# Kernel tuning notes

Measured on AMD Instinct MI355X. Metric: run time of the kernel, lower is better.

## Reference

```python
import jax, jax.numpy as jnp
import numpy as np

GROUPS = 8
NUM_HEADS = 4
EPS = 1e-5

def setup_inputs() -> dict:
    key = jax.random.key(0)
    k1, k2, k3 = jax.random.split(key, 3)
    B, C, H, W = 4, 128, 64, 64
    x = jax.random.normal(k1, (B, C, H, W), dtype=jnp.float32)
    gn_w = jnp.ones((C,), jnp.float32)
    gn_b = jnp.zeros((C,), jnp.float32)
    qkv_w = jax.random.normal(k2, (3 * C, C), dtype=jnp.float32) * (1.0 / np.sqrt(C))
    qkv_b = jnp.zeros((3 * C,), jnp.float32)
    proj_w = jax.random.normal(k3, (C, C), dtype=jnp.float32) * (1.0 / np.sqrt(C))
    proj_b = jnp.zeros((C,), jnp.float32)
    return {"x": x, "gn_w": gn_w, "gn_b": gn_b, "qkv_w": qkv_w,
            "qkv_b": qkv_b, "proj_w": proj_w, "proj_b": proj_b}

def group_norm(x, w, b):
    B, C, H, W = x.shape
    xg = x.reshape(B, GROUPS, C // GROUPS, H, W)
    mean = jnp.mean(xg, axis=(2, 3, 4), keepdims=True)
    var = jnp.var(xg, axis=(2, 3, 4), keepdims=True)
    xn = ((xg - mean) * jax.lax.rsqrt(var + EPS)).reshape(B, C, H, W)
    return xn * w[None, :, None, None] + b[None, :, None, None]

def reference(x, gn_w, gn_b, qkv_w, qkv_b, proj_w, proj_b):
    B, C, H, W = x.shape
    nh = NUM_HEADS
    hd = C // nh
    xn = group_norm(x, gn_w, gn_b)  # residual is the NORMALIZED x (torch code reassigns x)
    # 1x1 conv == channel matmul
    qkv = jnp.einsum('oc,bchw->bohw', qkv_w, xn) + qkv_b[None, :, None, None]
    qkv = qkv.reshape(B, 3, nh, hd, H * W)
    q, k, v = qkv[:, 0], qkv[:, 1], qkv[:, 2]          # [B, nh, hd, HW]
    attn = jnp.einsum('bhcd,bhce->bhde', q, k) * (C ** -0.5)  # note: full-C scale, as in torch code
    attn = jax.nn.softmax(attn, axis=-1)
    out = jnp.einsum('bhde,bhce->bhcd', attn, v).reshape(B, C, H, W)
    out = jnp.einsum('oc,bchw->bohw', proj_w, out) + proj_b[None, :, None, None]
    return out + xn
```

## Files before the change

### kernel.cpp

```cpp
#include <hip/hip_runtime.h>
#include <math.h>

#define BATCH 4
#define C 128
#define HW 4096
#define G 8
#define CPG 16
#define NH 4
#define HD 32
#define EPS 1e-5f
#define SCALE 0.08838834764831845f
#define LOG2E 1.44269504088896340f
#define GP 136

typedef unsigned int uint;
typedef unsigned short ushort;
typedef __attribute__((ext_vector_type(8))) short bf16x8;
typedef __attribute__((ext_vector_type(4))) float f32x4;

__device__ __forceinline__ ushort f2bf(float x) {
  uint u = __float_as_uint(x);
  u += 0x7fff + ((u >> 16) & 1);
  return (ushort)(u >> 16);
}
__device__ __forceinline__ ushort f2bf_r(float x) {
  return (ushort)((__float_as_uint(x) + 0x8000u) >> 16);
}
__device__ __forceinline__ float bf2f(ushort h) {
  return __uint_as_float(((uint)h) << 16);
}
__device__ __forceinline__ uint pk(float a, float b) {
#if __has_builtin(__builtin_amdgcn_cvt_pk_bf16_f32)
  auto r = __builtin_amdgcn_cvt_pk_bf16_f32(a, b);
  union { decltype(r) v; uint u; } x;
  x.v = r;
  return x.u;
#else
  uint ua = __float_as_uint(a) + 0x8000u;
  uint ub = __float_as_uint(b) + 0x8000u;
  return __builtin_amdgcn_perm(ub, ua, 0x07060302);
#endif
}
__device__ __forceinline__ bf16x8 as_bf(uint4 u) {
  union { uint4 a; bf16x8 b; } x; x.a = u; return x.b;
}
__device__ __forceinline__ float fexp2(float x) {
#if __has_builtin(__builtin_amdgcn_exp2f)
  return __builtin_amdgcn_exp2f(x);
#else
  return __exp2f(x);
#endif
}

__global__ __launch_bounds__(256) void gn_part(
    const float* __restrict__ x, float* __restrict__ stats) {
  const int bg = blockIdx.x >> 3, chunk = blockIdx.x & 7;
  const float* xp = x + (size_t)bg * (CPG * HW) + chunk * 8192;
  const int tid = threadIdx.x;
  float s = 0.f, ss = 0.f;
  #pragma unroll
  for (int j = 0; j < 8; j++) {
    float4 v = ((const float4*)xp)[j * 256 + tid];
    s += (v.x + v.y) + (v.z + v.w);
    ss += (v.x * v.x + v.y * v.y) + (v.z * v.z + v.w * v.w);
  }
  #pragma unroll
  for (int off = 32; off; off >>= 1) {
    s  += __shfl_down(s, off);
    ss += __shfl_down(ss, off);
  }
  __shared__ float rs[4], rss[4];
  const int lane = tid & 63, wid = tid >> 6;
  if (lane == 0) { rs[wid] = s; rss[wid] = ss; }
  __syncthreads();
  if (tid == 0) {
    stats[(bg * 8 + chunk) * 2]     = (rs[0] + rs[1]) + (rs[2] + rs[3]);
    stats[(bg * 8 + chunk) * 2 + 1] = (rss[0] + rss[1]) + (rss[2] + rss[3]);
  }
}

__device__ __forceinline__ void gn_coeff(
    const float* __restrict__ stats, const float* __restrict__ w,
    const float* __restrict__ b, int batch, int c, float& ca, float& cb) {
  const int bg = batch * G + (c >> 4);
  float s = 0.f, ss = 0.f;
  #pragma unroll
  for (int k = 0; k < 8; k++) {
    s  += stats[(bg * 8 + k) * 2];
    ss += stats[(bg * 8 + k) * 2 + 1];
  }
  const float mean = s * (1.0f / 65536.0f);
  const float var  = ss * (1.0f / 65536.0f) - mean * mean;
  const float inv  = rsqrtf(var + EPS);
  ca = w[c] * inv;
  cb = b[c] - mean * ca;
}

__global__ __launch_bounds__(256) void qkv_gemm(
    const float* __restrict__ x, const float* __restrict__ stats,
    const float* __restrict__ gnw, const float* __restrict__ gnb,
    const float* __restrict__ w, const float* __restrict__ bias,
    ushort* __restrict__ qkvb, ushort* __restrict__ kt) {
  const int b = blockIdx.z, my = blockIdx.y, n0 = blockIdx.x * 64;
  const int m0 = my * 128;
  const int tid = threadIdx.x, lane = tid & 63, wv = tid >> 6;
  const int li = lane & 15, g = lane >> 4;
  __shared__ ushort Ws[128][GP];
  __shared__ ushort Xs[64][GP];
  __shared__ float CA[C], CB[C];

  if (tid < C) gn_coeff(stats, gnw, gnb, b, tid, CA[tid], CB[tid]);
  __syncthreads();

  {
    const int row = tid >> 2, c0 = (tid & 3) * 32;
    #pragma unroll
    for (int mh = 0; mh < 2; mh++) {
      const float* wr = w + (size_t)(m0 + mh * 64 + row) * C + c0;
      #pragma unroll
      for (int k = 0; k < 4; k++) {
        float4 f0 = ((const float4*)wr)[k * 2];
        float4 f1 = ((const float4*)wr)[k * 2 + 1];
        uint4 u = {pk(f0.x, f0.y), pk(f0.z, f0.w), pk(f1.x, f1.y), pk(f1.z, f1.w)};
        *(uint4*)&Ws[mh * 64 + row][c0 + k * 8] = u;
      }
    }
  }
  {
    const int nX = tid & 63, c0 = (tid >> 6) * 32;
    const float* xb = x + (size_t)(b * C + c0) * HW + n0 + nX;
    #pragma unroll
    for (int k = 0; k < 4; k++) {
      float xv[8];
      #pragma unroll
      for (int j = 0; j < 8; j++) {
        int c = c0 + k * 8 + j;
        xv[j] = fmaf(xb[(size_t)(k * 8 + j) * HW], CA[c], CB[c]);
      }
      uint4 u = {pk(xv[0], xv[1]), pk(xv[2], xv[3]), pk(xv[4], xv[5]), pk(xv[6], xv[7])};
      *(uint4*)&Xs[nX][c0 + k * 8] = u;
    }
  }
  __syncthreads();

  f32x4 acc[2][4];
  #pragma unroll
  for (int mh = 0; mh < 2; mh++)
    #pragma unroll
    for (int nt = 0; nt < 4; nt++) acc[mh][nt] = (f32x4){0.f, 0.f, 0.f, 0.f};
  #pragma unroll
  for (int kk = 0; kk < 4; kk++) {
    bf16x8 af0 = *(const bf16x8*)&Ws[wv * 16 + li][kk * 32 + g * 8];
    bf16x8 af1 = *(const bf16x8*)&Ws[64 + wv * 16 + li][kk * 32 + g * 8];
    #pragma unroll
    for (int nt = 0; nt < 4; nt++) {
      bf16x8 bfr = *(const bf16x8*)&Xs[nt * 16 + li][kk * 32 + g * 8];
      acc[0][nt] = __builtin_amdgcn_mfma_f32_16x16x32_bf16(af0, bfr, acc[0][nt], 0, 0, 0);
      acc[1][nt] = __builtin_amdgcn_mfma_f32_16x16x32_bf16(af1, bfr, acc[1][nt], 0, 0, 0);
    }
  }
  #pragma unroll
  for (int mh = 0; mh < 2; mh++) {
    const int ob = m0 + mh * 64 + wv * 16 + g * 4;
    if (my == 1) {
      const int ck = ob - C;
      const int h  = ck >> 5;
      const int cl = ck & 31;
      ushort* ktp = kt + (size_t)(b * NH + h) * HW * HD;
      #pragma unroll
      for (int r = 0; r < 4; r++) {
        float bi = bias[ob + r];
        #pragma unroll
        for (int nt = 0; nt < 4; nt++) {
          int e = n0 + nt * 16 + li;
          ktp[(size_t)e * HD + cl + r] = f2bf(acc[mh][nt][r] + bi);
        }
      }
    } else {
      #pragma unroll
      for (int r = 0; r < 4; r++) {
        float bi = bias[ob + r];
        #pragma unroll
        for (int nt = 0; nt < 4; nt++) {
          qkvb[(size_t)(b * 3 * C + ob + r) * HW + n0 + nt * 16 + li] = f2bf(acc[mh][nt][r] + bi);
        }
      }
    }
  }
}

__global__ __launch_bounds__(512, 4) void attn_kernel(
    ushort* __restrict__ qkv, const ushort* __restrict__ kt) {
  const int bh = blockIdx.y, b = bh >> 2, h = bh & 3;
  const int tid = threadIdx.x, lane = tid & 63, wv = tid >> 6;
  const int li = lane & 15, g = lane >> 4;
  const int grp = wv >> 2, w4 = wv & 3;
  ushort* qp = qkv + (size_t)(b * 3 * C + h * HD) * HW;
  const ushort* vpl = qkv + (size_t)(b * 3 * C + 2 * C + h * HD) * HW;
  const ushort* ktp = kt + (size_t)bh * HW * HD;
  const int d0 = blockIdx.x * 128 + w4 * 32;

  __shared__ ushort Ks[2][2][32][40];
  __shared__ ushort Vs[2][2][32][40];
  __shared__ float OP[8][64][19];

  const float qs = SCALE * LOG2E;
  bf16x8 qf[2];
  #pragma unroll
  for (int dt = 0; dt < 2; dt++) {
    int d = d0 + dt * 16 + li;
    float qv[8];
    #pragma unroll
    for (int j = 0; j < 8; j++)
      qv[j] = bf2f(qp[(size_t)(g * 8 + j) * HW + d]) * qs;
    uint4 qu = {pk(qv[0], qv[1]), pk(qv[2], qv[3]), pk(qv[4], qv[5]), pk(qv[6], qv[7])};
    qf[dt] = as_bf(qu);
  }

  f32x4 O[2][2];
  #pragma unroll
  for (int dt = 0; dt < 2; dt++)
    #pragma unroll
    for (int ct = 0; ct < 2; ct++) O[dt][ct] = (f32x4){0.f, 0.f, 0.f, 0.f};
  f32x4 lacc[2] = {(f32x4){0.f, 0.f, 0.f, 0.f}, (f32x4){0.f, 0.f, 0.f, 0.f}};
  const uint one2 = 0x3F803F80u;
  const bf16x8 ones = as_bf((uint4){one2, one2, one2, one2});

  const int gt = tid & 255;
  const bool isK = gt < 128;
  const int t2 = gt & 127;
  const int srow = t2 >> 2, scol8 = (t2 & 3) * 8;
  const ushort* gK = ktp + (size_t)(grp * 64) * 1024 + t2 * 8;
  const ushort* gV = vpl + (size_t)srow * HW + grp * 2048 + scol8;

  uint4 st = isK ? *(const uint4*)&gK[0] : *(const uint4*)&gV[0];
  if (isK) *(uint4*)&Ks[grp][0][srow][scol8] = st;
  else     *(uint4*)&Vs[grp][0][srow][scol8] = st;
  st = isK ? *(const uint4*)&gK[1024] : *(const uint4*)&gV[32];
  __syncthreads();

  for (int it = 0; it < 64; it++) {
    const int cur = it & 1, nxt = cur ^ 1;
    if (isK) *(uint4*)&Ks[grp][nxt][srow][scol8] = st;
    else     *(uint4*)&Vs[grp][nxt][srow][scol8] = st;

    bf16x8 kf0 = *(const bf16x8*)&Ks[grp][cur][li][g * 8];
    bf16x8 kf1 = *(const bf16x8*)&Ks[grp][cur][16 + li][g * 8];
    uint2 va0 = *(const uint2*)&Vs[grp][cur][li][4 * g];
    uint2 va1 = *(const uint2*)&Vs[grp][cur][li][16 + 4 * g];
    uint2 vb0 = *(const uint2*)&Vs[grp][cur][16 + li][4 * g];
    uint2 vb1 = *(const uint2*)&Vs[grp][cur][16 + li][16 + 4 * g];
    bf16x8 vf0 = as_bf((uint4){va0.x, va0.y, va1.x, va1.y});
    bf16x8 vf1 = as_bf((uint4){vb0.x, vb0.y, vb1.x, vb1.y});

    const int tn = (it + 2) & 63;
    st = isK ? *(const uint4*)&gK[(size_t)tn * 1024] : *(const uint4*)&gV[tn * 32];

    const f32x4 z = (f32x4){0.f, 0.f, 0.f, 0.f};
    #pragma unroll
    for (int dt = 0; dt < 2; dt++) {
      f32x4 s0 = __builtin_amdgcn_mfma_f32_16x16x32_bf16(kf0, qf[dt], z, 0, 0, 0);
      f32x4 s1 = __builtin_amdgcn_mfma_f32_16x16x32_bf16(kf1, qf[dt], z, 0, 0, 0);
      float p0 = fexp2(s0[0]), p1 = fexp2(s0[1]), p2 = fexp2(s0[2]), p3 = fexp2(s0[3]);
      float p4 = fexp2(s1[0]), p5 = fexp2(s1[1]), p6 = fexp2(s1[2]), p7 = fexp2(s1[3]);
      uint4 pu = {pk(p0, p1), pk(p2, p3), pk(p4, p5), pk(p6, p7)};
      bf16x8 pf = as_bf(pu);
      lacc[dt] = __builtin_amdgcn_mfma_f32_16x16x32_bf16(ones, pf, lacc[dt], 0, 0, 0);
      O[dt][0] = __builtin_amdgcn_mfma_f32_16x16x32_bf16(vf0, pf, O[dt][0], 0, 0, 0);
      O[dt][1] = __builtin_amdgcn_mfma_f32_16x16x32_bf16(vf1, pf, O[dt][1], 0, 0, 0);
    }
    __syncthreads();
  }

  #pragma unroll
  for (int dt = 0; dt < 2; dt++) {
    #pragma unroll
    for (int ct = 0; ct < 2; ct++)
      #pragma unroll
      for (int r = 0; r < 4; r++) OP[wv][lane][dt * 8 + ct * 4 + r] = O[dt][ct][r];
    OP[wv][lane][16 + dt] = lacc[dt][0];
  }
  __syncthreads();
  const int pw = wv ^ 4;
  #pragma unroll
  for (int dt = 0; dt < 2; dt++) {
    const float inv = 1.0f / (lacc[dt][0] + OP[pw][lane][16 + dt]);
    const int d = d0 + dt * 16 + li;
    #pragma unroll
    for (int r = 0; r < 4; r++) {
      float val = O[dt][grp][r] + OP[pw][lane][dt * 8 + grp * 4 + r];
      qp[(size_t)(grp * 16 + g * 4 + r) * HW + d] = f2bf_r(val * inv);
    }
  }
}

__global__ __launch_bounds__(256) void proj_gemm(
    const ushort* __restrict__ qkvb, const float* __restrict__ w,
    const float* __restrict__ bias, const float* __restrict__ x,
    const float* __restrict__ stats, const float* __restrict__ gnw,
    const float* __restrict__ gnb, float* __restrict__ out) {
  const int b = blockIdx.z, m0 = blockIdx.y * 64, n0 = blockIdx.x * 64;
  const int tid = threadIdx.x, lane = tid & 63, wv = tid >> 6;
  const int li = lane & 15, g = lane >> 4;
  __shared__ ushort Ws[64][GP];
  __shared__ ushort Xs[64][GP];
  __shared__ float CA[64], CB[64];

  if (tid < 64) gn_coeff(stats, gnw, gnb, b, m0 + tid, CA[tid], CB[tid]);

  {
    const int row = tid >> 2, c0 = (tid & 3) * 32;
    const float* wr = w + (size_t)(m0 + row) * C + c0;
    #pragma unroll
    for (int k = 0; k < 4; k++) {
      float4 f0 = ((const float4*)wr)[k * 2];
      float4 f1 = ((const float4*)wr)[k * 2 + 1];
      uint4 u = {pk(f0.x, f0.y), pk(f0.z, f0.w), pk(f1.x, f1.y), pk(f1.z, f1.w)};
      *(uint4*)&Ws[row][c0 + k * 8] = u;
    }
  }
  {
    const int nX = tid & 63, c0 = (tid >> 6) * 32;
    const ushort* xb = qkvb + (size_t)(b * 3 * C + c0) * HW + n0 + nX;
    #pragma unroll
    for (int k = 0; k < 4; k++) {
      ushort t8[8];
      #pragma unroll
      for (int j = 0; j < 8; j++) t8[j] = xb[(size_t)(k * 8 + j) * HW];
      uint4 u;
      u.x = t8[0] | ((uint)t8[1] << 16);
      u.y = t8[2] | ((uint)t8[3] << 16);
      u.z = t8[4] | ((uint)t8[5] << 16);
      u.w = t8[6] | ((uint)t8[7] << 16);
      *(uint4*)&Xs[nX][c0 + k * 8] = u;
    }
  }
  __syncthreads();

  f32x4 acc[4];
  #pragma unroll
  for (int nt = 0; nt < 4; nt++) acc[nt] = (f32x4){0.f, 0.f, 0.f, 0.f};
  #pragma unroll
  for (int kk = 0; kk < 4; kk++) {
    bf16x8 af = *(const bf16x8*)&Ws[wv * 16 + li][kk * 32 + g * 8];
    #pragma unroll
    for (int nt = 0; nt < 4; nt++) {
      bf16x8 bfr = *(const bf16x8*)&Xs[nt * 16 + li][kk * 32 + g * 8];
      acc[nt] = __builtin_amdgcn_mfma_f32_16x16x32_bf16(af, bfr, acc[nt], 0, 0, 0);
    }
  }
  const int ob = m0 + wv * 16 + g * 4;
  #pragma unroll
  for (int r = 0; r < 4; r++) {
    const float bi = bias[ob + r];
    const float ca = CA[wv * 16 + g * 4 + r], cb = CB[wv * 16 + g * 4 + r];
    #pragma unroll
    for (int nt = 0; nt < 4; nt++) {
      size_t idx = (size_t)(b * C + ob + r) * HW + n0 + nt * 16 + li;
      out[idx] = acc[nt][r] + bi + fmaf(x[idx], ca, cb);
    }
  }
}

extern "C" void kernel_launch(void* const* d_in, const int* in_sizes, int n_in,
                              void* d_out, int out_size, void* d_ws, size_t ws_size,
                              hipStream_t stream) {
  const float* x     = (const float*)d_in[0];
  const float* gn_w  = (const float*)d_in[1];
  const float* gn_b  = (const float*)d_in[2];
  const float* qkv_w = (const float*)d_in[3];
  const float* qkv_b = (const float*)d_in[4];
  const float* pw    = (const float*)d_in[5];
  const float* pb    = (const float*)d_in[6];
  float* out = (float*)d_out;

  float*  stats = (float*)d_ws;
  ushort* qkvb  = (ushort*)((char*)d_ws + 4096);
  ushort* kt    = qkvb + (size_t)BATCH * 3 * C * HW;

  gn_part<<<dim3(256), dim3(256), 0, stream>>>(x, stats);
  qkv_gemm<<<dim3(HW / 64, 3, BATCH), dim3(256), 0, stream>>>(
      x, stats, gn_w, gn_b, qkv_w, qkv_b, qkvb, kt);
  attn_kernel<<<dim3(HW / 128, BATCH * NH), dim3(512), 0, stream>>>(qkvb, kt);
  proj_gemm<<<dim3(HW / 64, 2, BATCH), dim3(256), 0, stream>>>(
      qkvb, pw, pb, x, stats, gn_w, gn_b, out);
}
```

Baseline: 142.0 us.

## Permute V smem layout for single vector loads; widen proj_gemm tile to full C

```diff
diff --git a/kernel.cpp b/kernel.cpp
--- a/kernel.cpp
+++ b/kernel.cpp
@@ -230,28 +230,34 @@
   const bool isK = gt < 128;
   const int t2 = gt & 127;
   const int srow = t2 >> 2, scol8 = (t2 & 3) * 8;
+  const int q4 = t2 & 3;
+  const int p0 = 16 * (q4 & 1) + 4 * (q4 >> 1);
   const ushort* gK = ktp + (size_t)(grp * 64) * 1024 + t2 * 8;
   const ushort* gV = vpl + (size_t)srow * HW + grp * 2048 + scol8;
 
   uint4 st = isK ? *(const uint4*)&gK[0] : *(const uint4*)&gV[0];
-  if (isK) *(uint4*)&Ks[grp][0][srow][scol8] = st;
-  else     *(uint4*)&Vs[grp][0][srow][scol8] = st;
+  if (isK) {
+    *(uint4*)&Ks[grp][0][srow][scol8] = st;
+  } else {
+    *(uint2*)&Vs[grp][0][srow][p0]     = (uint2){st.x, st.y};
+    *(uint2*)&Vs[grp][0][srow][p0 + 8] = (uint2){st.z, st.w};
+  }
   st = isK ? *(const uint4*)&gK[1024] : *(const uint4*)&gV[32];
   __syncthreads();
 
   for (int it = 0; it < 64; it++) {
     const int cur = it & 1, nxt = cur ^ 1;
-    if (isK) *(uint4*)&Ks[grp][nxt][srow][scol8] = st;
-    else     *(uint4*)&Vs[grp][nxt][srow][scol8] = st;
+    if (isK) {
+      *(uint4*)&Ks[grp][nxt][srow][scol8] = st;
+    } else {
+      *(uint2*)&Vs[grp][nxt][srow][p0]     = (uint2){st.x, st.y};
+      *(uint2*)&Vs[grp][nxt][srow][p0 + 8] = (uint2){st.z, st.w};
+    }
 
     bf16x8 kf0 = *(const bf16x8*)&Ks[grp][cur][li][g * 8];
     bf16x8 kf1 = *(const bf16x8*)&Ks[grp][cur][16 + li][g * 8];
-    uint2 va0 = *(const uint2*)&Vs[grp][cur][li][4 * g];
-    uint2 va1 = *(const uint2*)&Vs[grp][cur][li][16 + 4 * g];
-    uint2 vb0 = *(const uint2*)&Vs[grp][cur][16 + li][4 * g];
-    uint2 vb1 = *(const uint2*)&Vs[grp][cur][16 + li][16 + 4 * g];
-    bf16x8 vf0 = as_bf((uint4){va0.x, va0.y, va1.x, va1.y});
-    bf16x8 vf1 = as_bf((uint4){vb0.x, vb0.y, vb1.x, vb1.y});
+    bf16x8 vf0 = *(const bf16x8*)&Vs[grp][cur][li][g * 8];
+    bf16x8 vf1 = *(const bf16x8*)&Vs[grp][cur][16 + li][g * 8];
 
     const int tn = (it + 2) & 63;
     st = isK ? *(const uint4*)&gK[(size_t)tn * 1024] : *(const uint4*)&gV[tn * 32];
@@ -261,9 +267,9 @@
     for (int dt = 0; dt < 2; dt++) {
       f32x4 s0 = __builtin_amdgcn_mfma_f32_16x16x32_bf16(kf0, qf[dt], z, 0, 0, 0);
       f32x4 s1 = __builtin_amdgcn_mfma_f32_16x16x32_bf16(kf1, qf[dt], z, 0, 0, 0);
-      float p0 = fexp2(s0[0]), p1 = fexp2(s0[1]), p2 = fexp2(s0[2]), p3 = fexp2(s0[3]);
-      float p4 = fexp2(s1[0]), p5 = fexp2(s1[1]), p6 = fexp2(s1[2]), p7 = fexp2(s1[3]);
-      uint4 pu = {pk(p0, p1), pk(p2, p3), pk(p4, p5), pk(p6, p7)};
+      float p0f = fexp2(s0[0]), p1f = fexp2(s0[1]), p2f = fexp2(s0[2]), p3f = fexp2(s0[3]);
+      float p4f = fexp2(s1[0]), p5f = fexp2(s1[1]), p6f = fexp2(s1[2]), p7f = fexp2(s1[3]);
+      uint4 pu = {pk(p0f, p1f), pk(p2f, p3f), pk(p4f, p5f), pk(p6f, p7f)};
       bf16x8 pf = as_bf(pu);
       lacc[dt] = __builtin_amdgcn_mfma_f32_16x16x32_bf16(ones, pf, lacc[dt], 0, 0, 0);
       O[dt][0] = __builtin_amdgcn_mfma_f32_16x16x32_bf16(vf0, pf, O[dt][0], 0, 0, 0);
@@ -299,24 +305,27 @@
     const float* __restrict__ bias, const float* __restrict__ x,
     const float* __restrict__ stats, const float* __restrict__ gnw,
     const float* __restrict__ gnb, float* __restrict__ out) {
-  const int b = blockIdx.z, m0 = blockIdx.y * 64, n0 = blockIdx.x * 64;
+  const int b = blockIdx.z, n0 = blockIdx.x * 64;
   const int tid = threadIdx.x, lane = tid & 63, wv = tid >> 6;
   const int li = lane & 15, g = lane >> 4;
-  __shared__ ushort Ws[64][GP];
+  __shared__ ushort Ws[128][GP];
   __shared__ ushort Xs[64][GP];
-  __shared__ float CA[64], CB[64];
-
-  if (tid < 64) gn_coeff(stats, gnw, gnb, b, m0 + tid, CA[tid], CB[tid]);
+  __shared__ float CA[C], CB[C];
+
+  if (tid < C) gn_coeff(stats, gnw, gnb, b, tid, CA[tid], CB[tid]);
 
   {
     const int row = tid >> 2, c0 = (tid & 3) * 32;
-    const float* wr = w + (size_t)(m0 + row) * C + c0;
-    #pragma unroll
-    for (int k = 0; k < 4; k++) {
-      float4 f0 = ((const float4*)wr)[k * 2];
-      float4 f1 = ((const float4*)wr)[k * 2 + 1];
-      uint4 u = {pk(f0.x, f0.y), pk(f0.z, f0.w), pk(f1.x, f1.y), pk(f1.z, f1.w)};
-      *(uint4*)&Ws[row][c0 + k * 8] = u;
+    #pragma unroll
+    for (int mh = 0; mh < 2; mh++) {
+      const float* wr = w + (size_t)(mh * 64 + row) * C + c0;
+      #pragma unroll
+      for (int k = 0; k < 4; k++) {
+        float4 f0 = ((const float4*)wr)[k * 2];
+        float4 f1 = ((const float4*)wr)[k * 2 + 1];
+        uint4 u = {pk(f0.x, f0.y), pk(f0.z, f0.w), pk(f1.x, f1.y), pk(f1.z, f1.w)};
+        *(uint4*)&Ws[mh * 64 + row][c0 + k * 8] = u;
+      }
     }
   }
   {
@@ -337,27 +346,34 @@
   }
   __syncthreads();
 
-  f32x4 acc[4];
-  #pragma unroll
-  for (int nt = 0; nt < 4; nt++) acc[nt] = (f32x4){0.f, 0.f, 0.f, 0.f};
+  f32x4 acc[2][4];
+  #pragma unroll
+  for (int mh = 0; mh < 2; mh++)
+    #pragma unroll
+    for (int nt = 0; nt < 4; nt++) acc[mh][nt] = (f32x4){0.f, 0.f, 0.f, 0.f};
   #pragma unroll
   for (int kk = 0; kk < 4; kk++) {
-    bf16x8 af = *(const bf16x8*)&Ws[wv * 16 + li][kk * 32 + g * 8];
+    bf16x8 af0 = *(const bf16x8*)&Ws[wv * 16 + li][kk * 32 + g * 8];
+    bf16x8 af1 = *(const bf16x8*)&Ws[64 + wv * 16 + li][kk * 32 + g * 8];
     #pragma unroll
     for (int nt = 0; nt < 4; nt++) {
       bf16x8 bfr = *(const bf16x8*)&Xs[nt * 16 + li][kk * 32 + g * 8];
-      acc[nt] = __builtin_amdgcn_mfma_f32_16x16x32_bf16(af, bfr, acc[nt], 0, 0, 0);
-    }
-  }
-  const int ob = m0 + wv * 16 + g * 4;
-  #pragma unroll
-  for (int r = 0; r < 4; r++) {
-    const float bi = bias[ob + r];
-    const float ca = CA[wv * 16 + g * 4 + r], cb = CB[wv * 16 + g * 4 + r];
-    #pragma unroll
-    for (int nt = 0; nt < 4; nt++) {
-      size_t idx = (size_t)(b * C + ob + r) * HW + n0 + nt * 16 + li;
-      out[idx] = acc[nt][r] + bi + fmaf(x[idx], ca, cb);
+      acc[0][nt] = __builtin_amdgcn_mfma_f32_16x16x32_bf16(af0, bfr, acc[0][nt], 0, 0, 0);
+      acc[1][nt] = __builtin_amdgcn_mfma_f32_16x16x32_bf16(af1, bfr, acc[1][nt], 0, 0, 0);
+    }
+  }
+  #pragma unroll
+  for (int mh = 0; mh < 2; mh++) {
+    const int ob = mh * 64 + wv * 16 + g * 4;
+    #pragma unroll
+    for (int r = 0; r < 4; r++) {
+      const float bi = bias[ob + r];
+      const float ca = CA[ob + r], cb = CB[ob + r];
+      #pragma unroll
+      for (int nt = 0; nt < 4; nt++) {
+        size_t idx = (size_t)(b * C + ob + r) * HW + n0 + nt * 16 + li;
+        out[idx] = acc[mh][nt][r] + bi + fmaf(x[idx], ca, cb);
+      }
     }
   }
 }
@@ -382,6 +398,6 @@
   qkv_gemm<<<dim3(HW / 64, 3, BATCH), dim3(256), 0, stream>>>(
       x, stats, gn_w, gn_b, qkv_w, qkv_b, qkvb, kt);
   attn_kernel<<<dim3(HW / 128, BATCH * NH), dim3(512), 0, stream>>>(qkvb, kt);
-  proj_gemm<<<dim3(HW / 64, 2, BATCH), dim3(256), 0, stream>>>(
+  proj_gemm<<<dim3(HW / 64, 1, BATCH), dim3(256), 0, stream>>>(
       qkvb, pw, pb, x, stats, gn_w, gn_b, out);
 }
```

Measured after the change: 141.7 us. Within noise of the previous version (-0.2%).
